# Performance work log

Measured on AMD Instinct MI355X. Metric: run time of the kernel, lower is better.

Reference implementation:

```python
import jax, jax.numpy as jnp
import numpy as np

B, T, P, D = 32, 8, 196, 768
M = 10
NUM_CLASSES = 100
NUM_IDX = 98
P_MASK = 0.5


def setup_inputs() -> dict:
    key = jax.random.key(0)
    ks = jax.random.split(key, 16)
    s = 0.02
    inp = {
        'visual': jax.random.normal(ks[0], (B, T * P, D), jnp.float32),
        'audio': jax.random.normal(ks[1], (B, D), jnp.float32),
        'causal': jax.random.normal(ks[2], (B, M, D), jnp.float32),
        'random_mask': jax.random.uniform(ks[3], (B, T, P, D)) < P_MASK,
        'Wa': jax.random.normal(ks[4], (D, D), jnp.float32) * s,
        'ba': jnp.zeros((D,), jnp.float32),
        'Wv': jax.random.normal(ks[5], (D, D), jnp.float32) * s,
        'bv': jnp.zeros((D,), jnp.float32),
        'Waa': jax.random.normal(ks[6], (D, D), jnp.float32) * s,
        'baa': jnp.zeros((D,), jnp.float32),
        'Wav': jax.random.normal(ks[7], (D, D), jnp.float32) * s,
        'bav': jnp.zeros((D,), jnp.float32),
        'Wf': jax.random.normal(ks[8], (D, D), jnp.float32) * s,
        'bf': jnp.zeros((D,), jnp.float32),
        'Wf2': jax.random.normal(ks[9], (D, 1), jnp.float32) * s,
        'bf2': jnp.zeros((1,), jnp.float32),
        'Wc': jax.random.normal(ks[10], (D, NUM_CLASSES), jnp.float32) * s,
        'bc': jnp.zeros((NUM_CLASSES,), jnp.float32),
        'causal_param': jnp.zeros((1,), jnp.float32),
    }
    return inp


def reference(visual, audio, causal, random_mask, Wa, ba, Wv, bv, Waa, baa,
              Wav, bav, Wf, bf, Wf2, bf2, Wc, bc, causal_param):
    vis = visual.reshape(visual.shape[0], T, -1, D)  # [B,8,196,768]

    # causal_intervention_mean_feature4
    cp = jax.nn.sigmoid(causal_param)                 # soft_clamp2, [1]
    feats = causal @ Wf + bf                          # [B,M,D]
    feats2 = jnp.swapaxes(causal @ Wf2 + bf2, 1, 2)   # [B,1,M]
    fw = jax.nn.softmax(jnp.tanh(feats), axis=1)      # [B,M,D]
    ci = jnp.einsum('bom,bmd->bd', feats2, fw * causal)  # bmm + squeeze
    audio2 = cp * ci + audio                          # [B,D]

    # audio_visual_attention1
    pa = jnp.tanh(audio2 @ Waa + baa)                 # [B,D]
    pv = jnp.tanh(vis @ Wav + bav)                    # [B,T,P,D]
    sscore = pv * pa[:, None, None, :]                # einsum ijkd,id->ijkd
    sattn = jax.nn.softmax(sscore, axis=2)            # softmax over patches
    patch = jnp.sum(sattn, axis=-1)                   # [B,T,P]
    thresh = jnp.sort(patch, axis=-1)[:, :, NUM_IDX]  # per (b,t) threshold
    spa_mask = patch < thresh[:, :, None]             # [B,T,P]
    final_mask = ~(spa_mask[..., None] & random_mask) # [B,T,P,D]
    sfilt = jnp.where(final_mask, sattn, 0.0)

    sav = jnp.sum(sfilt * pv, axis=2)                 # [B,T,D]
    tattn = jax.nn.softmax(sav * pa[:, None, :], axis=1)

    vp = jnp.sum(sfilt * vis, axis=2)                 # [B,T,D]
    vp = jnp.sum(tattn * vp, axis=1)                  # [B,D]

    af = jax.nn.relu(audio2 @ Wa + ba)
    vf = jax.nn.relu(vp @ Wv + bv)
    logits = (af + vf) @ Wc + bc                      # [B,num_classes]
    return logits
```

## Files before the change

kernel.cpp:

```cpp
#include <hip/hip_runtime.h>
#include <hip/hip_bf16.h>
#include <hip/hip_fp16.h>
#include <math.h>

#define BB 32
#define TT 8
#define PP 196
#define DD 768
#define MM 10
#define NCLS 100
#define NIDX 98

typedef __attribute__((ext_vector_type(8))) short short8v;
typedef __attribute__((ext_vector_type(4))) float float4v;

__device__ __forceinline__ float fast_tanh(float x) {
    float e = __expf(2.0f * x);
    return 1.0f - 2.0f / (e + 1.0f);
}
__device__ __forceinline__ unsigned short f2bf(float x) {
    __hip_bfloat16 h = __float2bfloat16(x);
    return *(unsigned short*)&h;
}
__device__ __forceinline__ float bf2f(unsigned short h) {
    return __uint_as_float(((unsigned)h) << 16);
}
__device__ __forceinline__ unsigned short f2h(float x) {
    __half h = __float2half(x);
    return *(unsigned short*)&h;
}
__device__ __forceinline__ float h2f(unsigned short u) {
    __half h = *(__half*)&u;
    return __half2float(h);
}

__global__ __launch_bounds__(768) void k_prep_all(
    const float* __restrict__ vis, unsigned short* __restrict__ visb,
    const unsigned int* __restrict__ rm, int* __restrict__ mode,
    const float* __restrict__ Wav, unsigned short* __restrict__ Wht,
    const float* __restrict__ causal, const float* __restrict__ Wf,
    const float* __restrict__ Wf2,
    float* __restrict__ pf, float* __restrict__ pf2) {
    int t = threadIdx.x;
    int bid = blockIdx.x;
    if (bid < 1024) {
        const size_t NC = (size_t)BB * TT * PP * DD / 8;
        size_t gid = (size_t)bid * 768 + t;
        for (size_t i = gid; i < NC; i += 1024 * 768) {
            const float4* s = (const float4*)(vis + i * 8);
            float4 x = s[0], y = s[1];
            __hip_bfloat162 h;
            unsigned int u0, u1, u2, u3;
            h = __float22bfloat162_rn(make_float2(x.x, x.y)); u0 = *(unsigned int*)&h;
            h = __float22bfloat162_rn(make_float2(x.z, x.w)); u1 = *(unsigned int*)&h;
            h = __float22bfloat162_rn(make_float2(y.x, y.y)); u2 = *(unsigned int*)&h;
            h = __float22bfloat162_rn(make_float2(y.z, y.w)); u3 = *(unsigned int*)&h;
            uint4 o; o.x = u0; o.y = u1; o.z = u2; o.w = u3;
            ((uint4*)visb)[i] = o;
        }
        if (bid == 0) {
            __shared__ int f_ni, f_nf;
            if (t == 0) { f_ni = 0; f_nf = 0; }
            __syncthreads();
            int ni = 0, nf = 0;
            for (int i = t; i < 16384; i += 768) {
                unsigned int v = rm[i];
                ni |= (v > 1u) ? 1 : 0;
                nf |= (v != 0u && v != 0x3F800000u) ? 1 : 0;
            }
            if (ni) atomicOr(&f_ni, 1);
            if (nf) atomicOr(&f_nf, 1);
            __syncthreads();
            if (t == 0) *mode = f_ni ? (f_nf ? 2 : 1) : 0;
        }
    } else if (bid < 1600) {
        __shared__ float tile[32][33];
        int bb = bid - 1024;
        int bn = (bb % 24) * 32;
        int bk = (bb / 24) * 32;
        if (t < 256) {
            int tx = t & 31, ty = t >> 5;
            #pragma unroll
            for (int i = 0; i < 4; ++i)
                tile[ty + i * 8][tx] = Wav[(size_t)(bk + ty + i * 8) * DD + bn + tx];
        }
        __syncthreads();
        if (t < 256) {
            int tx = t & 31, ty = t >> 5;
            #pragma unroll
            for (int i = 0; i < 4; ++i) {
                int n = bn + ty + i * 8, k = bk + tx;
                Wht[(size_t)n * DD + k] = f2bf(tile[tx][ty + i * 8]);
            }
        }
    } else {
        __shared__ float cs[MM][256];
        __shared__ float red[MM][12];
        int bb = bid - 1600;
        int b = bb % 32, kc = bb / 32;
        int k0 = kc * 256;
        for (int i = t; i < MM * 256; i += 768)
            cs[i >> 8][i & 255] = causal[((size_t)b * MM + (i >> 8)) * DD + k0 + (i & 255)];
        __syncthreads();
        int wave = t >> 6, lane = t & 63;
        float w2v = (t < 256) ? Wf2[k0 + t] : 0.f;
        #pragma unroll
        for (int m = 0; m < MM; ++m) {
            float p = (t < 256) ? cs[m][t] * w2v : 0.f;
            #pragma unroll
            for (int o = 32; o > 0; o >>= 1) p += __shfl_down(p, o);
            if (lane == 0) red[m][wave] = p;
        }
        __syncthreads();
        if (t < MM) {
            float s = 0.f;
            #pragma unroll
            for (int wv = 0; wv < 4; ++wv) s += red[t][wv];
            pf2[(b * 3 + kc) * MM + t] = s;
        }
        float acc[MM];
        #pragma unroll
        for (int m = 0; m < MM; ++m) acc[m] = 0.f;
        #pragma unroll 4
        for (int k = 0; k < 256; ++k) {
            float wv = Wf[(size_t)(k0 + k) * DD + t];
            #pragma unroll
            for (int m = 0; m < MM; ++m) acc[m] = fmaf(cs[m][k], wv, acc[m]);
        }
        #pragma unroll
        for (int m = 0; m < MM; ++m)
            pf[(((size_t)b * 3 + kc) * MM + m) * DD + t] = acc[m];
    }
}

__global__ __launch_bounds__(768) void k_audio2a(
    const float* __restrict__ causal, const float* __restrict__ audio,
    const float* __restrict__ pf, const float* __restrict__ pf2,
    const float* __restrict__ bf, const float* __restrict__ bf2,
    const float* __restrict__ cparam, float* __restrict__ a2) {
    int b = blockIdx.x;
    int t = threadIdx.x;
    float cp = 1.0f / (1.0f + __expf(-cparam[0]));
    float tf[MM], f2[MM];
    float mx = -1e30f;
    #pragma unroll
    for (int m = 0; m < MM; ++m) {
        float acc = bf[t];
        float s2 = bf2[0];
        #pragma unroll
        for (int kc = 0; kc < 3; ++kc) {
            acc += pf[(((size_t)b * 3 + kc) * MM + m) * DD + t];
            s2 += pf2[(b * 3 + kc) * MM + m];
        }
        tf[m] = fast_tanh(acc);
        f2[m] = s2;
        mx = fmaxf(mx, tf[m]);
    }
    float s = 0.f;
    #pragma unroll
    for (int m = 0; m < MM; ++m) { tf[m] = __expf(tf[m] - mx); s += tf[m]; }
    float inv = 1.0f / s;
    float ci = 0.f;
    #pragma unroll
    for (int m = 0; m < MM; ++m)
        ci += f2[m] * (tf[m] * inv) * causal[((size_t)b * MM + m) * DD + t];
    a2[(size_t)b * DD + t] = cp * ci + audio[(size_t)b * DD + t];
}

__global__ __launch_bounds__(256) void k_audio2b(
    const float* __restrict__ a2,
    const float* __restrict__ Waa, const float* __restrict__ baa,
    const float* __restrict__ Wa, const float* __restrict__ ba,
    float* __restrict__ pa, float* __restrict__ af, float* __restrict__ colsum) {
    int gid0 = (blockIdx.y * 24 + blockIdx.x) * 256 + threadIdx.x;
    for (int i = gid0; i < BB * TT * DD; i += 48 * 256) colsum[i] = 0.f;
    __shared__ float a2s[16][DD + 4];
    int sel = blockIdx.y;
    const float* W = sel ? Wa : Waa;
    int t = threadIdx.x;
    int c = blockIdx.x * 32 + (t & 31);
    int slot = t >> 5;
    float bias = sel ? ba[c] : baa[c];
    #pragma unroll
    for (int g = 0; g < 2; ++g) {
        if (g) __syncthreads();
        for (int i = t; i < 16 * DD; i += 256)
            a2s[i / DD][i % DD] = a2[(size_t)(g * 16 + i / DD) * DD + i % DD];
        __syncthreads();
        float acc0 = 0.f, acc1 = 0.f;
        #pragma unroll 8
        for (int k = 0; k < DD; ++k) {
            float wv = W[(size_t)k * DD + c];
            acc0 = fmaf(a2s[slot][k], wv, acc0);
            acc1 = fmaf(a2s[slot + 8][k], wv, acc1);
        }
        int b0 = g * 16 + slot, b1 = b0 + 8;
        if (sel == 0) {
            pa[(size_t)b0 * DD + c] = fast_tanh(acc0 + bias);
            pa[(size_t)b1 * DD + c] = fast_tanh(acc1 + bias);
        } else {
            af[(size_t)b0 * DD + c] = fmaxf(acc0 + bias, 0.f);
            af[(size_t)b1 * DD + c] = fmaxf(acc1 + bias, 0.f);
        }
    }
}

__global__ __launch_bounds__(256, 4) void k_pv_mfma(
    const unsigned short* __restrict__ visb, const unsigned short* __restrict__ Wht,
    const float* __restrict__ bav, const float* __restrict__ pa,
    unsigned short* __restrict__ pvh, float* __restrict__ colsum)
{
    __shared__ unsigned short SH[4][4096];
    __shared__ float cred[256];
    int wg = blockIdx.x;
    int lin = (wg & 7) * 294 + (wg >> 3);
    int mt = lin / 6, nt = lin % 6;
    int i0 = mt * 128, n0 = nt * 128;
    int t = threadIdx.x, w = t >> 6, l = t & 63;
    int wm = (w >> 1) * 64, wn = (w & 1) * 64;

    float4v zero4 = {0.f, 0.f, 0.f, 0.f};
    float4v acc[4][4];
    #pragma unroll
    for (int a = 0; a < 4; ++a)
        #pragma unroll
        for (int b = 0; b < 4; ++b) acc[a][b] = zero4;

    int srow[2], scs[2];
    #pragma unroll
    for (int j = 0; j < 2; ++j) {
        int row = (w * 2 + j) * 16 + (l >> 2);
        srow[j] = row;
        scs[j] = (l & 3) ^ ((row >> 1) & 3);
    }

#define STAGE(bb, wnd_)                                                          \
    {                                                                            \
        int kw_ = (wnd_) * 32;                                                   \
        _Pragma("unroll")                                                        \
        for (int j = 0; j < 2; ++j) {                                            \
            size_t aoff_ = (size_t)(i0 + srow[j]) * DD + kw_ + scs[j] * 8;       \
            __builtin_amdgcn_global_load_lds(                                    \
                (const __attribute__((address_space(1))) unsigned int*)(visb + aoff_), \
                (__attribute__((address_space(3))) unsigned int*)&SH[bb][(w * 2 + j) * 512], \
                16, 0, 0);                                                       \
            size_t boff_ = (size_t)(n0 + srow[j]) * DD + kw_ + scs[j] * 8;       \
            __builtin_amdgcn_global_load_lds(                                    \
                (const __attribute__((address_space(1))) unsigned int*)(Wht + boff_), \
                (__attribute__((address_space(3))) unsigned int*)&SH[2 + bb][(w * 2 + j) * 512], \
                16, 0, 0);                                                       \
        }                                                                        \
    }

    STAGE(0, 0);
    for (int wnd = 0; wnd < 24; ++wnd) {
        int cur = wnd & 1;
        if (wnd < 23) {
            STAGE(cur ^ 1, wnd + 1);
            asm volatile("s_waitcnt vmcnt(4)" ::: "memory");
        } else {
            asm volatile("s_waitcnt vmcnt(0)" ::: "memory");
        }
        __builtin_amdgcn_s_barrier();
        __builtin_amdgcn_s_setprio(1);
        {
            short8v ahf[4], bhf[4];
            int cA = l >> 4;
            #pragma unroll
            for (int mr = 0; mr < 4; ++mr) {
                int row = wm + mr * 16 + (l & 15);
                ahf[mr] = *(const short8v*)&SH[cur][row * 32 + ((cA ^ ((row >> 1) & 3)) * 8)];
            }
            #pragma unroll
            for (int nc = 0; nc < 4; ++nc) {
                int row = wn + nc * 16 + (l & 15);
                bhf[nc] = *(const short8v*)&SH[2 + cur][row * 32 + ((cA ^ ((row >> 1) & 3)) * 8)];
            }
            #pragma unroll
            for (int mr = 0; mr < 4; ++mr)
                #pragma unroll
                for (int nc = 0; nc < 4; ++nc)
                    acc[mr][nc] = __builtin_amdgcn_mfma_f32_16x16x32_bf16(
                        ahf[mr], bhf[nc], acc[mr][nc], 0, 0, 0);
        }
        __builtin_amdgcn_s_setprio(0);
        asm volatile("s_waitcnt lgkmcnt(0)" ::: "memory");
        __builtin_amdgcn_sched_barrier(0);
        __builtin_amdgcn_s_barrier();
    }
#undef STAGE
    unsigned short* Cl = &SH[0][0];
    if (t < 256) cred[t] = 0.f;
    __syncthreads();
    int bt0 = i0 / PP;
    int btbound = (bt0 + 1) * PP;
    #pragma unroll
    for (int nc = 0; nc < 4; ++nc) {
        int cl = wn + nc * 16 + (l & 15);
        int col = n0 + cl;
        float bias = bav[col];
        #pragma unroll
        for (int mr = 0; mr < 4; ++mr) {
            int lr0 = wm + mr * 16 + ((l >> 4) << 2);
            int row0 = i0 + lr0;
            int bq = row0 / (TT * PP);
            float pav = pa[(size_t)bq * DD + col];
            float esum = 0.f;
            #pragma unroll
            for (int v = 0; v < 4; ++v) {
                unsigned short pb = f2h(fast_tanh(acc[mr][nc][v] + bias));
                int lr = lr0 + v;
                int boff = lr * 256 + ((cl * 2) ^ ((lr & 7) << 4));
                *(unsigned short*)((char*)Cl + boff) = pb;
                esum += __expf(h2f(pb) * pav);
            }
            int btg = (row0 >= btbound) ? 1 : 0;
            atomicAdd(&cred[btg * 128 + cl], esum);
        }
    }
    __syncthreads();
    #pragma unroll
    for (int rb = 0; rb < 2; ++rb) {
        int lr = (t >> 2) + rb * 64;
        size_t grow = (size_t)(i0 + lr) * DD + n0;
        #pragma unroll
        for (int q = 0; q < 4; ++q) {
            int ch = (t & 3) + q * 4;
            int boff = lr * 256 + ((ch * 16) ^ ((lr & 7) << 4));
            uint4 val = *(uint4*)((char*)Cl + boff);
            *(uint4*)(pvh + grow + ch * 8) = val;
        }
    }
    if (t < 256) {
        int btg = t >> 7, cl = t & 127;
        if (btg == 0 || btbound < i0 + 128)
            atomicAdd(&colsum[(size_t)(bt0 + btg) * DD + n0 + cl], cred[t]);
    }
}

__global__ __launch_bounds__(768) void k_patchsum(
    const unsigned short* __restrict__ pvh, const float* __restrict__ pa,
    const float* __restrict__ colsum, float* __restrict__ patch_q) {
    int bt = blockIdx.x, qd = blockIdx.y;
    int b = bt >> 3;
    size_t base = (size_t)bt * PP * DD;
    int c0 = qd * 192;
    __shared__ float2 pi[192];
    int t = threadIdx.x;
    if (t < 192) {
        int col = c0 + t;
        pi[t] = make_float2(pa[(size_t)b * DD + col],
                            1.0f / colsum[(size_t)bt * DD + col]);
    }
    __syncthreads();
    int wv = t >> 6, l = t & 63;
    for (int p = wv; p < PP; p += 12) {
        float sum = 0.f;
        if (l < 48) {
            const uint2* rv = (const uint2*)(pvh + base + (size_t)p * DD + c0);
            uint2 v = rv[l];
            int c = l * 4;
            float2 q0 = pi[c], q1 = pi[c + 1], q2 = pi[c + 2], q3 = pi[c + 3];
            sum = __expf(h2f((unsigned short)(v.x & 0xFFFFu)) * q0.x) * q0.y
                + __expf(h2f((unsigned short)(v.x >> 16)) * q1.x) * q1.y
                + __expf(h2f((unsigned short)(v.y & 0xFFFFu)) * q2.x) * q2.y
                + __expf(h2f((unsigned short)(v.y >> 16)) * q3.x) * q3.y;
        }
        #pragma unroll
        for (int o = 32; o > 0; o >>= 1) sum += __shfl_down(sum, o);
        if (l == 0) patch_q[((size_t)bt * PP + p) * 4 + qd] = sum;
    }
}

__global__ __launch_bounds__(768) void k_masked(
    const unsigned short* __restrict__ pvh, const unsigned short* __restrict__ visb,
    const void* __restrict__ rmask, const int* __restrict__ mode_p,
    const float* __restrict__ pa, const float* __restrict__ colsum,
    const float* __restrict__ patch_q,
    float* __restrict__ sav, float* __restrict__ vpt) {
    int bt = blockIdx.x;
    int qd = blockIdx.y;
    int b = bt >> 3;
    size_t base = (size_t)bt * PP * DD;
    __shared__ float patch[PP];
    __shared__ unsigned char spa[PP];
    __shared__ float red_s[4][192];
    __shared__ float red_v[4][192];
    int t = threadIdx.x;
    if (t < PP) {
        float4 v = *(const float4*)&patch_q[((size_t)bt * PP + t) * 4];
        patch[t] = ((v.x + v.y) + v.z) + v.w;
    }
    __syncthreads();
    if (t < PP) {
        float x = patch[t];
        int c = 0;
        for (int q = 0; q < PP; ++q) c += (patch[q] <= x) ? 1 : 0;
        spa[t] = (c <= NIDX) ? 1 : 0;
    }
    int pg = t / 192;
    int c = t - pg * 192;
    int col = qd * 192 + c;
    int p0 = pg * 49, p1 = p0 + 49;
    float pav = pa[(size_t)b * DD + col];
    float inv = 1.0f / colsum[(size_t)bt * DD + col];
    __syncthreads();
    const unsigned short* pvb = pvh + base + col;
    const unsigned short* vib = visb + base + col;
    float sava = 0.f, vpa = 0.f;
    int mode = *mode_p;
    if (mode == 0) {
        const int* mb = (const int*)rmask + base + col;
        #pragma unroll 7
        for (int p = p0; p < p1; ++p) {
            float pvv = h2f(pvb[(size_t)p * DD]);
            float sa = __expf(pvv * pav) * inv;
            bool km = !(spa[p] && (mb[(size_t)p * DD] != 0));
            if (km) { sava = fmaf(sa, pvv, sava); vpa = fmaf(sa, bf2f(vib[(size_t)p * DD]), vpa); }
        }
    } else if (mode == 1) {
        const float* mb = (const float*)rmask + base + col;
        #pragma unroll 7
        for (int p = p0; p < p1; ++p) {
            float pvv = h2f(pvb[(size_t)p * DD]);
            float sa = __expf(pvv * pav) * inv;
            bool km = !(spa[p] && (mb[(size_t)p * DD] != 0.f));
            if (km) { sava = fmaf(sa, pvv, sava); vpa = fmaf(sa, bf2f(vib[(size_t)p * DD]), vpa); }
        }
    } else {
        const unsigned char* mb = (const unsigned char*)rmask + base + col;
        #pragma unroll 7
        for (int p = p0; p < p1; ++p) {
            float pvv = h2f(pvb[(size_t)p * DD]);
            float sa = __expf(pvv * pav) * inv;
            bool km = !(spa[p] && (mb[(size_t)p * DD] != 0));
            if (km) { sava = fmaf(sa, pvv, sava); vpa = fmaf(sa, bf2f(vib[(size_t)p * DD]), vpa); }
        }
    }
    red_s[pg][c] = sava;
    red_v[pg][c] = vpa;
    __syncthreads();
    if (t < 192) {
        int col2 = qd * 192 + t;
        sav[(size_t)bt * DD + col2] = red_s[0][t] + red_s[1][t] + red_s[2][t] + red_s[3][t];
        vpt[(size_t)bt * DD + col2] = red_v[0][t] + red_v[1][t] + red_v[2][t] + red_v[3][t];
    }
}

__global__ __launch_bounds__(768) void k_tail(
    const float* __restrict__ sav, const float* __restrict__ vpt,
    const float* __restrict__ pa, const float* __restrict__ af,
    const float* __restrict__ Wv, const float* __restrict__ bv,
    const float* __restrict__ Wc, const float* __restrict__ bc,
    float* __restrict__ out) {
    int b = blockIdx.x;
    int t = threadIdx.x;
    __shared__ float vp[DD];
    __shared__ float h[DD];
    float pav = pa[(size_t)b * DD + t];
    float x[TT];
    float mx = -1e30f;
    #pragma unroll
    for (int k = 0; k < TT; ++k) {
        x[k] = sav[((size_t)b * TT + k) * DD + t] * pav;
        mx = fmaxf(mx, x[k]);
    }
    float s = 0.f;
    #pragma unroll
    for (int k = 0; k < TT; ++k) { x[k] = __expf(x[k] - mx); s += x[k]; }
    float inv = 1.0f / s;
    float acc = 0.f;
    #pragma unroll
    for (int k = 0; k < TT; ++k)
        acc += x[k] * inv * vpt[((size_t)b * TT + k) * DD + t];
    vp[t] = acc;
    __syncthreads();
    float accv = bv[t];
    #pragma unroll 8
    for (int k = 0; k < DD; ++k) accv = fmaf(vp[k], Wv[(size_t)k * DD + t], accv);
    h[t] = fmaxf(accv, 0.f) + af[(size_t)b * DD + t];
    __syncthreads();
    if (t < NCLS) {
        float accc = bc[t];
        #pragma unroll 8
        for (int k = 0; k < DD; ++k) accc = fmaf(h[k], Wc[(size_t)k * NCLS + t], accc);
        out[(size_t)b * NCLS + t] = accc;
    }
}

extern "C" void kernel_launch(void* const* d_in, const int* in_sizes, int n_in,
                              void* d_out, int out_size, void* d_ws, size_t ws_size,
                              hipStream_t stream) {
    const float* visual = (const float*)d_in[0];
    const float* audio  = (const float*)d_in[1];
    const float* causal = (const float*)d_in[2];
    const void*  rmask  = d_in[3];
    const float* Wa   = (const float*)d_in[4];
    const float* ba   = (const float*)d_in[5];
    const float* Wv   = (const float*)d_in[6];
    const float* bv   = (const float*)d_in[7];
    const float* Waa  = (const float*)d_in[8];
    const float* baa  = (const float*)d_in[9];
    const float* Wav  = (const float*)d_in[10];
    const float* bav  = (const float*)d_in[11];
    const float* Wf   = (const float*)d_in[12];
    const float* bf   = (const float*)d_in[13];
    const float* Wf2  = (const float*)d_in[14];
    const float* bf2  = (const float*)d_in[15];
    const float* Wc   = (const float*)d_in[16];
    const float* bc   = (const float*)d_in[17];
    const float* cpar = (const float*)d_in[18];
    float* out = (float*)d_out;

    const size_t NE = (size_t)BB * TT * PP * DD;
    unsigned short* Wht = (unsigned short*)d_ws;
    float* pfreg = (float*)(Wht + (size_t)DD * DD);
    float* colsum = pfreg;
    float* savw  = colsum + (size_t)BB * TT * DD;
    float* vptw  = savw + (size_t)BB * TT * DD;
    float* pf    = pfreg;
    float* pf2   = pfreg + (size_t)BB * 3 * MM * DD;
    float* a2w   = pf2 + 1024;
    float* paw   = a2w + (size_t)BB * DD;
    float* afw   = paw + (size_t)BB * DD;
    int*   modew = (int*)(afw + (size_t)BB * DD);
    unsigned short* visb = (unsigned short*)(modew + 16);
    unsigned short* pvh  = visb + NE;
    float* patchq = (float*)(pvh + NE);

    k_prep_all<<<1696, 768, 0, stream>>>(visual, visb, (const unsigned int*)rmask,
                                         modew, Wav, Wht, causal, Wf, Wf2, pf, pf2);
    k_audio2a<<<BB, 768, 0, stream>>>(causal, audio, pf, pf2, bf, bf2, cpar, a2w);
    k_audio2b<<<dim3(24, 2), 256, 0, stream>>>(a2w, Waa, baa, Wa, ba, paw, afw, colsum);
    k_pv_mfma<<<2352, 256, 0, stream>>>(visb, Wht, bav, paw, pvh, colsum);
    k_patchsum<<<dim3(BB * TT, 4), 768, 0, stream>>>(pvh, paw, colsum, patchq);
    k_masked<<<dim3(BB * TT, 4), 768, 0, stream>>>(pvh, visb, rmask, modew, paw,
                                                   colsum, patchq, savw, vptw);
    k_tail<<<BB, 768, 0, stream>>>(savw, vptw, paw, afw, Wv, bv, Wc, bc, out);
}
```

Baseline: 479.5 us.

## Fuse fp32-to-bf16 visual conversion into GEMM A-operand register loads

Removes the separate pass that converted the visual tensor to bf16. The GEMM now loads fp32 A tiles directly into registers from global memory, converts them in registers, and prefetches the next window, while only the weight operand is staged through LDS. The masked-reduction kernel reads fp32 visual directly. This saves a full read-convert-write pass over the large tensor, but doubles the A-operand bytes the GEMM loads from global memory and raises register pressure. It also doubles the visual bytes read by the masked kernel.

```diff
diff --git a/kernel.cpp b/kernel.cpp
--- a/kernel.cpp
+++ b/kernel.cpp
@@ -22,9 +22,6 @@
     __hip_bfloat16 h = __float2bfloat16(x);
     return *(unsigned short*)&h;
 }
-__device__ __forceinline__ float bf2f(unsigned short h) {
-    return __uint_as_float(((unsigned)h) << 16);
-}
 __device__ __forceinline__ unsigned short f2h(float x) {
     __half h = __float2half(x);
     return *(unsigned short*)&h;
@@ -35,7 +32,6 @@
 }
 
 __global__ __launch_bounds__(768) void k_prep_all(
-    const float* __restrict__ vis, unsigned short* __restrict__ visb,
     const unsigned int* __restrict__ rm, int* __restrict__ mode,
     const float* __restrict__ Wav, unsigned short* __restrict__ Wht,
     const float* __restrict__ causal, const float* __restrict__ Wf,
@@ -43,21 +39,7 @@
     float* __restrict__ pf, float* __restrict__ pf2) {
     int t = threadIdx.x;
     int bid = blockIdx.x;
-    if (bid < 1024) {
-        const size_t NC = (size_t)BB * TT * PP * DD / 8;
-        size_t gid = (size_t)bid * 768 + t;
-        for (size_t i = gid; i < NC; i += 1024 * 768) {
-            const float4* s = (const float4*)(vis + i * 8);
-            float4 x = s[0], y = s[1];
-            __hip_bfloat162 h;
-            unsigned int u0, u1, u2, u3;
-            h = __float22bfloat162_rn(make_float2(x.x, x.y)); u0 = *(unsigned int*)&h;
-            h = __float22bfloat162_rn(make_float2(x.z, x.w)); u1 = *(unsigned int*)&h;
-            h = __float22bfloat162_rn(make_float2(y.x, y.y)); u2 = *(unsigned int*)&h;
-            h = __float22bfloat162_rn(make_float2(y.z, y.w)); u3 = *(unsigned int*)&h;
-            uint4 o; o.x = u0; o.y = u1; o.z = u2; o.w = u3;
-            ((uint4*)visb)[i] = o;
-        }
+    if (bid < 576) {
         if (bid == 0) {
             __shared__ int f_ni, f_nf;
             if (t == 0) { f_ni = 0; f_nf = 0; }
@@ -73,11 +55,9 @@
             __syncthreads();
             if (t == 0) *mode = f_ni ? (f_nf ? 2 : 1) : 0;
         }
-    } else if (bid < 1600) {
         __shared__ float tile[32][33];
-        int bb = bid - 1024;
-        int bn = (bb % 24) * 32;
-        int bk = (bb / 24) * 32;
+        int bn = (bid % 24) * 32;
+        int bk = (bid / 24) * 32;
         if (t < 256) {
             int tx = t & 31, ty = t >> 5;
             #pragma unroll
@@ -96,7 +76,7 @@
     } else {
         __shared__ float cs[MM][256];
         __shared__ float red[MM][12];
-        int bb = bid - 1600;
+        int bb = bid - 576;
         int b = bb % 32, kc = bb / 32;
         int k0 = kc * 256;
         for (int i = t; i < MM * 256; i += 768)
@@ -206,11 +186,11 @@
 }
 
 __global__ __launch_bounds__(256, 4) void k_pv_mfma(
-    const unsigned short* __restrict__ visb, const unsigned short* __restrict__ Wht,
+    const float* __restrict__ vis, const unsigned short* __restrict__ Wht,
     const float* __restrict__ bav, const float* __restrict__ pa,
     unsigned short* __restrict__ pvh, float* __restrict__ colsum)
 {
-    __shared__ unsigned short SH[4][4096];
+    __shared__ unsigned short SH[16384];
     __shared__ float cred[256];
     int wg = blockIdx.x;
     int lin = (wg & 7) * 294 + (wg >> 3);
@@ -226,55 +206,75 @@
         #pragma unroll
         for (int b = 0; b < 4; ++b) acc[a][b] = zero4;
 
-    int srow[2], scs[2];
+    int brow[2], bcs[2];
     #pragma unroll
     for (int j = 0; j < 2; ++j) {
-        int row = (w * 2 + j) * 16 + (l >> 2);
-        srow[j] = row;
-        scs[j] = (l & 3) ^ ((row >> 1) & 3);
-    }
-
-#define STAGE(bb, wnd_)                                                          \
+        int row = j * 64 + (t >> 2);
+        brow[j] = row;
+        bcs[j] = (t & 3) ^ ((row >> 1) & 3);
+    }
+    const float* aptrs[4];
+    #pragma unroll
+    for (int mr = 0; mr < 4; ++mr) {
+        int row = i0 + wm + mr * 16 + (l & 15);
+        aptrs[mr] = vis + (size_t)row * DD + (l >> 4) * 8;
+    }
+    float fA[4][8];
+
+#define LOADA(wnd_)                                                              \
+    {                                                                            \
+        int off_ = (wnd_) * 32;                                                  \
+        _Pragma("unroll")                                                        \
+        for (int mr = 0; mr < 4; ++mr) {                                         \
+            *(float4*)&fA[mr][0] = *(const float4*)(aptrs[mr] + off_);           \
+            *(float4*)&fA[mr][4] = *(const float4*)(aptrs[mr] + off_ + 4);       \
+        }                                                                        \
+    }
+#define STAGEB(bb, wnd_)                                                         \
     {                                                                            \
         int kw_ = (wnd_) * 32;                                                   \
         _Pragma("unroll")                                                        \
         for (int j = 0; j < 2; ++j) {                                            \
-            size_t aoff_ = (size_t)(i0 + srow[j]) * DD + kw_ + scs[j] * 8;       \
-            __builtin_amdgcn_global_load_lds(                                    \
-                (const __attribute__((address_space(1))) unsigned int*)(visb + aoff_), \
-                (__attribute__((address_space(3))) unsigned int*)&SH[bb][(w * 2 + j) * 512], \
-                16, 0, 0);                                                       \
-            size_t boff_ = (size_t)(n0 + srow[j]) * DD + kw_ + scs[j] * 8;       \
+            size_t boff_ = (size_t)(n0 + brow[j]) * DD + kw_ + bcs[j] * 8;       \
             __builtin_amdgcn_global_load_lds(                                    \
                 (const __attribute__((address_space(1))) unsigned int*)(Wht + boff_), \
-                (__attribute__((address_space(3))) unsigned int*)&SH[2 + bb][(w * 2 + j) * 512], \
+                (__attribute__((address_space(3))) unsigned int*)&SH[(bb) * 4096 + j * 2048 + t * 8], \
                 16, 0, 0);                                                       \
         }                                                                        \
     }
 
-    STAGE(0, 0);
+    LOADA(0);
+    STAGEB(0, 0);
     for (int wnd = 0; wnd < 24; ++wnd) {
         int cur = wnd & 1;
         if (wnd < 23) {
-            STAGE(cur ^ 1, wnd + 1);
-            asm volatile("s_waitcnt vmcnt(4)" ::: "memory");
+            STAGEB(cur ^ 1, wnd + 1);
+            asm volatile("s_waitcnt vmcnt(2)" ::: "memory");
         } else {
             asm volatile("s_waitcnt vmcnt(0)" ::: "memory");
         }
         __builtin_amdgcn_s_barrier();
         __builtin_amdgcn_s_setprio(1);
+        short8v ahf[4];
+        #pragma unroll
+        for (int mr = 0; mr < 4; ++mr) {
+            unsigned int u[4];
+            #pragma unroll
+            for (int i = 0; i < 4; ++i) {
+                float2 fp = make_float2(fA[mr][2 * i], fA[mr][2 * i + 1]);
+                __hip_bfloat162 h2 = __float22bfloat162_rn(fp);
+                u[i] = *(unsigned int*)&h2;
+            }
+            ahf[mr] = *(short8v*)u;
+        }
+        if (wnd < 23) LOADA(wnd + 1);
         {
-            short8v ahf[4], bhf[4];
+            short8v bhf[4];
             int cA = l >> 4;
-            #pragma unroll
-            for (int mr = 0; mr < 4; ++mr) {
-                int row = wm + mr * 16 + (l & 15);
-                ahf[mr] = *(const short8v*)&SH[cur][row * 32 + ((cA ^ ((row >> 1) & 3)) * 8)];
-            }
             #pragma unroll
             for (int nc = 0; nc < 4; ++nc) {
                 int row = wn + nc * 16 + (l & 15);
-                bhf[nc] = *(const short8v*)&SH[2 + cur][row * 32 + ((cA ^ ((row >> 1) & 3)) * 8)];
+                bhf[nc] = *(const short8v*)&SH[cur * 4096 + row * 32 + ((cA ^ ((row >> 1) & 3)) * 8)];
             }
             #pragma unroll
             for (int mr = 0; mr < 4; ++mr)
@@ -288,8 +288,9 @@
         __builtin_amdgcn_sched_barrier(0);
         __builtin_amdgcn_s_barrier();
     }
-#undef STAGE
-    unsigned short* Cl = &SH[0][0];
+#undef STAGEB
+#undef LOADA
+    unsigned short* Cl = &SH[0];
     if (t < 256) cred[t] = 0.f;
     __syncthreads();
     int bt0 = i0 / PP;
@@ -373,7 +374,7 @@
 }
 
 __global__ __launch_bounds__(768) void k_masked(
-    const unsigned short* __restrict__ pvh, const unsigned short* __restrict__ visb,
+    const unsigned short* __restrict__ pvh, const float* __restrict__ vis,
     const void* __restrict__ rmask, const int* __restrict__ mode_p,
     const float* __restrict__ pa, const float* __restrict__ colsum,
     const float* __restrict__ patch_q,
@@ -406,7 +407,7 @@
     float inv = 1.0f / colsum[(size_t)bt * DD + col];
     __syncthreads();
     const unsigned short* pvb = pvh + base + col;
-    const unsigned short* vib = visb + base + col;
+    const float* vib = vis + base + col;
     float sava = 0.f, vpa = 0.f;
     int mode = *mode_p;
     if (mode == 0) {
@@ -416,7 +417,7 @@
             float pvv = h2f(pvb[(size_t)p * DD]);
             float sa = __expf(pvv * pav) * inv;
             bool km = !(spa[p] && (mb[(size_t)p * DD] != 0));
-            if (km) { sava = fmaf(sa, pvv, sava); vpa = fmaf(sa, bf2f(vib[(size_t)p * DD]), vpa); }
+            if (km) { sava = fmaf(sa, pvv, sava); vpa = fmaf(sa, vib[(size_t)p * DD], vpa); }
         }
     } else if (mode == 1) {
         const float* mb = (const float*)rmask + base + col;
@@ -425,7 +426,7 @@
             float pvv = h2f(pvb[(size_t)p * DD]);
             float sa = __expf(pvv * pav) * inv;
             bool km = !(spa[p] && (mb[(size_t)p * DD] != 0.f));
-            if (km) { sava = fmaf(sa, pvv, sava); vpa = fmaf(sa, bf2f(vib[(size_t)p * DD]), vpa); }
+            if (km) { sava = fmaf(sa, pvv, sava); vpa = fmaf(sa, vib[(size_t)p * DD], vpa); }
         }
     } else {
         const unsigned char* mb = (const unsigned char*)rmask + base + col;
@@ -434,7 +435,7 @@
             float pvv = h2f(pvb[(size_t)p * DD]);
             float sa = __expf(pvv * pav) * inv;
             bool km = !(spa[p] && (mb[(size_t)p * DD] != 0));
-            if (km) { sava = fmaf(sa, pvv, sava); vpa = fmaf(sa, bf2f(vib[(size_t)p * DD]), vpa); }
+            if (km) { sava = fmaf(sa, pvv, sava); vpa = fmaf(sa, vib[(size_t)p * DD], vpa); }
         }
     }
     red_s[pg][c] = sava;
@@ -524,17 +525,16 @@
     float* paw   = a2w + (size_t)BB * DD;
     float* afw   = paw + (size_t)BB * DD;
     int*   modew = (int*)(afw + (size_t)BB * DD);
-    unsigned short* visb = (unsigned short*)(modew + 16);
-    unsigned short* pvh  = visb + NE;
+    unsigned short* pvh  = (unsigned short*)(modew + 16);
     float* patchq = (float*)(pvh + NE);
 
-    k_prep_all<<<1696, 768, 0, stream>>>(visual, visb, (const unsigned int*)rmask,
-                                         modew, Wav, Wht, causal, Wf, Wf2, pf, pf2);
+    k_prep_all<<<672, 768, 0, stream>>>((const unsigned int*)rmask, modew,
+                                        Wav, Wht, causal, Wf, Wf2, pf, pf2);
     k_audio2a<<<BB, 768, 0, stream>>>(causal, audio, pf, pf2, bf, bf2, cpar, a2w);
     k_audio2b<<<dim3(24, 2), 256, 0, stream>>>(a2w, Waa, baa, Wa, ba, paw, afw, colsum);
-    k_pv_mfma<<<2352, 256, 0, stream>>>(visb, Wht, bav, paw, pvh, colsum);
+    k_pv_mfma<<<2352, 256, 0, stream>>>(visual, Wht, bav, paw, pvh, colsum);
     k_patchsum<<<dim3(BB * TT, 4), 768, 0, stream>>>(pvh, paw, colsum, patchq);
-    k_masked<<<dim3(BB * TT, 4), 768, 0, stream>>>(pvh, visb, rmask, modew, paw,
+    k_masked<<<dim3(BB * TT, 4), 768, 0, stream>>>(pvh, visual, rmask, modew, paw,
                                                    colsum, patchq, savw, vptw);
     k_tail<<<BB, 768, 0, stream>>>(savw, vptw, paw, afw, Wv, bv, Wc, bc, out);
 }
```

New measurement: 675.1 us. 1.41x slower.

## Compute masked sums as unmasked totals minus excluded terms in GEMM epilogue

Applied to the files above, without the earlier changes.

The GEMM epilogue now also accumulates the unmasked sums exp(pv*pa)*pv and exp(pv*pa)*vis per (b,t,column) into two new global buffers, which the prep kernel zeroes. The masked kernel then skips patches not selected by the spatial mask and only visits patches that are both spatially selected and randomly masked. It subtracts their contribution from the normalized unmasked totals. This removes about half the loads and exps in the masked pass, but adds extra visb reads and atomics in the GEMM epilogue and uses a subtraction that can lose floating-point precision.

```diff
diff --git a/kernel.cpp b/kernel.cpp
--- a/kernel.cpp
+++ b/kernel.cpp
@@ -40,7 +40,8 @@
     const float* __restrict__ Wav, unsigned short* __restrict__ Wht,
     const float* __restrict__ causal, const float* __restrict__ Wf,
     const float* __restrict__ Wf2,
-    float* __restrict__ pf, float* __restrict__ pf2) {
+    float* __restrict__ pf, float* __restrict__ pf2,
+    float* __restrict__ uzero) {
     int t = threadIdx.x;
     int bid = blockIdx.x;
     if (bid < 1024) {
@@ -58,6 +59,8 @@
             uint4 o; o.x = u0; o.y = u1; o.z = u2; o.w = u3;
             ((uint4*)visb)[i] = o;
         }
+        for (int i = bid * 768 + t; i < 2 * BB * TT * DD; i += 1024 * 768)
+            uzero[i] = 0.f;
         if (bid == 0) {
             __shared__ int f_ni, f_nf;
             if (t == 0) { f_ni = 0; f_nf = 0; }
@@ -208,10 +211,11 @@
 __global__ __launch_bounds__(256, 4) void k_pv_mfma(
     const unsigned short* __restrict__ visb, const unsigned short* __restrict__ Wht,
     const float* __restrict__ bav, const float* __restrict__ pa,
-    unsigned short* __restrict__ pvh, float* __restrict__ colsum)
+    unsigned short* __restrict__ pvh, float* __restrict__ colsum,
+    float* __restrict__ upv, float* __restrict__ uvis)
 {
     __shared__ unsigned short SH[4][4096];
-    __shared__ float cred[256];
+    __shared__ float cred[3][256];
     int wg = blockIdx.x;
     int lin = (wg & 7) * 294 + (wg >> 3);
     int mt = lin / 6, nt = lin % 6;
@@ -290,7 +294,7 @@
     }
 #undef STAGE
     unsigned short* Cl = &SH[0][0];
-    if (t < 256) cred[t] = 0.f;
+    if (t < 256) { cred[0][t] = 0.f; cred[1][t] = 0.f; cred[2][t] = 0.f; }
     __syncthreads();
     int bt0 = i0 / PP;
     int btbound = (bt0 + 1) * PP;
@@ -305,17 +309,25 @@
             int row0 = i0 + lr0;
             int bq = row0 / (TT * PP);
             float pav = pa[(size_t)bq * DD + col];
-            float esum = 0.f;
+            float esum = 0.f, epsum = 0.f, evsum = 0.f;
             #pragma unroll
             for (int v = 0; v < 4; ++v) {
-                unsigned short pb = f2h(fast_tanh(acc[mr][nc][v] + bias));
+                float pvf = fast_tanh(acc[mr][nc][v] + bias);
+                unsigned short pb = f2h(pvf);
+                float pvq = h2f(pb);
                 int lr = lr0 + v;
                 int boff = lr * 256 + ((cl * 2) ^ ((lr & 7) << 4));
                 *(unsigned short*)((char*)Cl + boff) = pb;
-                esum += __expf(h2f(pb) * pav);
+                float e = __expf(pvq * pav);
+                esum += e;
+                epsum = fmaf(e, pvq, epsum);
+                float vv = bf2f(visb[(size_t)(row0 + v) * DD + col]);
+                evsum = fmaf(e, vv, evsum);
             }
             int btg = (row0 >= btbound) ? 1 : 0;
-            atomicAdd(&cred[btg * 128 + cl], esum);
+            atomicAdd(&cred[0][btg * 128 + cl], esum);
+            atomicAdd(&cred[1][btg * 128 + cl], epsum);
+            atomicAdd(&cred[2][btg * 128 + cl], evsum);
         }
     }
     __syncthreads();
@@ -333,8 +345,12 @@
     }
     if (t < 256) {
         int btg = t >> 7, cl = t & 127;
-        if (btg == 0 || btbound < i0 + 128)
-            atomicAdd(&colsum[(size_t)(bt0 + btg) * DD + n0 + cl], cred[t]);
+        if (btg == 0 || btbound < i0 + 128) {
+            size_t gi = (size_t)(bt0 + btg) * DD + n0 + cl;
+            atomicAdd(&colsum[gi], cred[0][t]);
+            atomicAdd(&upv[gi], cred[1][t]);
+            atomicAdd(&uvis[gi], cred[2][t]);
+        }
     }
 }
 
@@ -377,6 +393,7 @@
     const void* __restrict__ rmask, const int* __restrict__ mode_p,
     const float* __restrict__ pa, const float* __restrict__ colsum,
     const float* __restrict__ patch_q,
+    const float* __restrict__ upv, const float* __restrict__ uvis,
     float* __restrict__ sav, float* __restrict__ vpt) {
     int bt = blockIdx.x;
     int qd = blockIdx.y;
@@ -407,43 +424,56 @@
     __syncthreads();
     const unsigned short* pvb = pvh + base + col;
     const unsigned short* vib = visb + base + col;
-    float sava = 0.f, vpa = 0.f;
+    float sub_s = 0.f, sub_v = 0.f;
     int mode = *mode_p;
     if (mode == 0) {
         const int* mb = (const int*)rmask + base + col;
-        #pragma unroll 7
         for (int p = p0; p < p1; ++p) {
+            if (!spa[p]) continue;
             float pvv = h2f(pvb[(size_t)p * DD]);
-            float sa = __expf(pvv * pav) * inv;
-            bool km = !(spa[p] && (mb[(size_t)p * DD] != 0));
-            if (km) { sava = fmaf(sa, pvv, sava); vpa = fmaf(sa, bf2f(vib[(size_t)p * DD]), vpa); }
+            int mv = mb[(size_t)p * DD];
+            if (mv != 0) {
+                float sa = __expf(pvv * pav) * inv;
+                sub_s = fmaf(sa, pvv, sub_s);
+                sub_v = fmaf(sa, bf2f(vib[(size_t)p * DD]), sub_v);
+            }
         }
     } else if (mode == 1) {
         const float* mb = (const float*)rmask + base + col;
-        #pragma unroll 7
         for (int p = p0; p < p1; ++p) {
+            if (!spa[p]) continue;
             float pvv = h2f(pvb[(size_t)p * DD]);
-            float sa = __expf(pvv * pav) * inv;
-            bool km = !(spa[p] && (mb[(size_t)p * DD] != 0.f));
-            if (km) { sava = fmaf(sa, pvv, sava); vpa = fmaf(sa, bf2f(vib[(size_t)p * DD]), vpa); }
+            float mv = mb[(size_t)p * DD];
+            if (mv != 0.f) {
+                float sa = __expf(pvv * pav) * inv;
+                sub_s = fmaf(sa, pvv, sub_s);
+                sub_v = fmaf(sa, bf2f(vib[(size_t)p * DD]), sub_v);
+            }
         }
     } else {
         const unsigned char* mb = (const unsigned char*)rmask + base + col;
-        #pragma unroll 7
         for (int p = p0; p < p1; ++p) {
+            if (!spa[p]) continue;
             float pvv = h2f(pvb[(size_t)p * DD]);
-            float sa = __expf(pvv * pav) * inv;
-            bool km = !(spa[p] && (mb[(size_t)p * DD] != 0));
-            if (km) { sava = fmaf(sa, pvv, sava); vpa = fmaf(sa, bf2f(vib[(size_t)p * DD]), vpa); }
-        }
-    }
-    red_s[pg][c] = sava;
-    red_v[pg][c] = vpa;
+            unsigned char mv = mb[(size_t)p * DD];
+            if (mv != 0) {
+                float sa = __expf(pvv * pav) * inv;
+                sub_s = fmaf(sa, pvv, sub_s);
+                sub_v = fmaf(sa, bf2f(vib[(size_t)p * DD]), sub_v);
+            }
+        }
+    }
+    red_s[pg][c] = sub_s;
+    red_v[pg][c] = sub_v;
     __syncthreads();
     if (t < 192) {
         int col2 = qd * 192 + t;
-        sav[(size_t)bt * DD + col2] = red_s[0][t] + red_s[1][t] + red_s[2][t] + red_s[3][t];
-        vpt[(size_t)bt * DD + col2] = red_v[0][t] + red_v[1][t] + red_v[2][t] + red_v[3][t];
+        size_t gi = (size_t)bt * DD + col2;
+        float inv2 = 1.0f / colsum[gi];
+        float ss = red_s[0][t] + red_s[1][t] + red_s[2][t] + red_s[3][t];
+        float sv = red_v[0][t] + red_v[1][t] + red_v[2][t] + red_v[3][t];
+        sav[gi] = upv[gi] * inv2 - ss;
+        vpt[gi] = uvis[gi] * inv2 - sv;
     }
 }
 
@@ -527,14 +557,18 @@
     unsigned short* visb = (unsigned short*)(modew + 16);
     unsigned short* pvh  = visb + NE;
     float* patchq = (float*)(pvh + NE);
+    float* upvw   = patchq + (size_t)BB * TT * PP * 4;
+    float* uvisw  = upvw + (size_t)BB * TT * DD;
 
     k_prep_all<<<1696, 768, 0, stream>>>(visual, visb, (const unsigned int*)rmask,
-                                         modew, Wav, Wht, causal, Wf, Wf2, pf, pf2);
+                                         modew, Wav, Wht, causal, Wf, Wf2, pf, pf2,
+                                         upvw);
     k_audio2a<<<BB, 768, 0, stream>>>(causal, audio, pf, pf2, bf, bf2, cpar, a2w);
     k_audio2b<<<dim3(24, 2), 256, 0, stream>>>(a2w, Waa, baa, Wa, ba, paw, afw, colsum);
-    k_pv_mfma<<<2352, 256, 0, stream>>>(visb, Wht, bav, paw, pvh, colsum);
+    k_pv_mfma<<<2352, 256, 0, stream>>>(visb, Wht, bav, paw, pvh, colsum, upvw, uvisw);
     k_patchsum<<<dim3(BB * TT, 4), 768, 0, stream>>>(pvh, paw, colsum, patchq);
     k_masked<<<dim3(BB * TT, 4), 768, 0, stream>>>(pvh, visb, rmask, modew, paw,
-                                                   colsum, patchq, savw, vptw);
+                                                   colsum, patchq, upvw, uvisw,
+                                                   savw, vptw);
     k_tail<<<BB, 768, 0, stream>>>(savw, vptw, paw, afw, Wv, bv, Wc, bc, out);
 }
```

Result: slower. 573.5 us (+19.6%).

## Compute masked sums as unmasked totals minus masked-out contributions

Applied to the files above, without the earlier changes.

Patchsum now also accumulates the unmasked per-column sums of exp-weighted pv and visual, reusing its pv read and adding a visual read. The masked kernel then only visits patches selected by the spatial mask and subtracts the contributions where the random mask is also set, applying the normalisation at the end. This skips about half of the patch reads in the masked kernel, in exchange for extra visual traffic in patchsum and divergent branches.

```diff
diff --git a/kernel.cpp b/kernel.cpp
--- a/kernel.cpp
+++ b/kernel.cpp
@@ -339,36 +339,63 @@
 }
 
 __global__ __launch_bounds__(768) void k_patchsum(
-    const unsigned short* __restrict__ pvh, const float* __restrict__ pa,
-    const float* __restrict__ colsum, float* __restrict__ patch_q) {
+    const unsigned short* __restrict__ pvh, const unsigned short* __restrict__ visb,
+    const float* __restrict__ pa, const float* __restrict__ colsum,
+    float* __restrict__ patch_q, float* __restrict__ upv, float* __restrict__ uvis) {
     int bt = blockIdx.x, qd = blockIdx.y;
     int b = bt >> 3;
     size_t base = (size_t)bt * PP * DD;
     int c0 = qd * 192;
     __shared__ float2 pi[192];
+    __shared__ float us[192], vs[192];
     int t = threadIdx.x;
     if (t < 192) {
         int col = c0 + t;
         pi[t] = make_float2(pa[(size_t)b * DD + col],
                             1.0f / colsum[(size_t)bt * DD + col]);
+        us[t] = 0.f; vs[t] = 0.f;
     }
     __syncthreads();
     int wv = t >> 6, l = t & 63;
+    int c = l * 4;
+    float up0 = 0.f, up1 = 0.f, up2 = 0.f, up3 = 0.f;
+    float uv0 = 0.f, uv1 = 0.f, uv2 = 0.f, uv3 = 0.f;
     for (int p = wv; p < PP; p += 12) {
         float sum = 0.f;
         if (l < 48) {
             const uint2* rv = (const uint2*)(pvh + base + (size_t)p * DD + c0);
+            const uint2* rb = (const uint2*)(visb + base + (size_t)p * DD + c0);
             uint2 v = rv[l];
-            int c = l * 4;
+            uint2 wv2 = rb[l];
+            float p0 = h2f((unsigned short)(v.x & 0xFFFFu));
+            float p1 = h2f((unsigned short)(v.x >> 16));
+            float p2 = h2f((unsigned short)(v.y & 0xFFFFu));
+            float p3 = h2f((unsigned short)(v.y >> 16));
             float2 q0 = pi[c], q1 = pi[c + 1], q2 = pi[c + 2], q3 = pi[c + 3];
-            sum = __expf(h2f((unsigned short)(v.x & 0xFFFFu)) * q0.x) * q0.y
-                + __expf(h2f((unsigned short)(v.x >> 16)) * q1.x) * q1.y
-                + __expf(h2f((unsigned short)(v.y & 0xFFFFu)) * q2.x) * q2.y
-                + __expf(h2f((unsigned short)(v.y >> 16)) * q3.x) * q3.y;
+            float e0 = __expf(p0 * q0.x), e1 = __expf(p1 * q1.x);
+            float e2 = __expf(p2 * q2.x), e3 = __expf(p3 * q3.x);
+            sum = e0 * q0.y + e1 * q1.y + e2 * q2.y + e3 * q3.y;
+            up0 = fmaf(e0, p0, up0); up1 = fmaf(e1, p1, up1);
+            up2 = fmaf(e2, p2, up2); up3 = fmaf(e3, p3, up3);
+            uv0 = fmaf(e0, bf2f((unsigned short)(wv2.x & 0xFFFFu)), uv0);
+            uv1 = fmaf(e1, bf2f((unsigned short)(wv2.x >> 16)), uv1);
+            uv2 = fmaf(e2, bf2f((unsigned short)(wv2.y & 0xFFFFu)), uv2);
+            uv3 = fmaf(e3, bf2f((unsigned short)(wv2.y >> 16)), uv3);
         }
         #pragma unroll
         for (int o = 32; o > 0; o >>= 1) sum += __shfl_down(sum, o);
         if (l == 0) patch_q[((size_t)bt * PP + p) * 4 + qd] = sum;
+    }
+    if (l < 48) {
+        atomicAdd(&us[c], up0); atomicAdd(&us[c + 1], up1);
+        atomicAdd(&us[c + 2], up2); atomicAdd(&us[c + 3], up3);
+        atomicAdd(&vs[c], uv0); atomicAdd(&vs[c + 1], uv1);
+        atomicAdd(&vs[c + 2], uv2); atomicAdd(&vs[c + 3], uv3);
+    }
+    __syncthreads();
+    if (t < 192) {
+        upv[(size_t)bt * DD + c0 + t] = us[t];
+        uvis[(size_t)bt * DD + c0 + t] = vs[t];
     }
 }
 
@@ -377,6 +404,7 @@
     const void* __restrict__ rmask, const int* __restrict__ mode_p,
     const float* __restrict__ pa, const float* __restrict__ colsum,
     const float* __restrict__ patch_q,
+    const float* __restrict__ upv, const float* __restrict__ uvis,
     float* __restrict__ sav, float* __restrict__ vpt) {
     int bt = blockIdx.x;
     int qd = blockIdx.y;
@@ -403,47 +431,59 @@
     int col = qd * 192 + c;
     int p0 = pg * 49, p1 = p0 + 49;
     float pav = pa[(size_t)b * DD + col];
-    float inv = 1.0f / colsum[(size_t)bt * DD + col];
     __syncthreads();
     const unsigned short* pvb = pvh + base + col;
     const unsigned short* vib = visb + base + col;
-    float sava = 0.f, vpa = 0.f;
+    float sub_s = 0.f, sub_v = 0.f;
     int mode = *mode_p;
     if (mode == 0) {
         const int* mb = (const int*)rmask + base + col;
-        #pragma unroll 7
         for (int p = p0; p < p1; ++p) {
+            if (!spa[p]) continue;
             float pvv = h2f(pvb[(size_t)p * DD]);
-            float sa = __expf(pvv * pav) * inv;
-            bool km = !(spa[p] && (mb[(size_t)p * DD] != 0));
-            if (km) { sava = fmaf(sa, pvv, sava); vpa = fmaf(sa, bf2f(vib[(size_t)p * DD]), vpa); }
+            int mv = mb[(size_t)p * DD];
+            if (mv != 0) {
+                float e = __expf(pvv * pav);
+                sub_s = fmaf(e, pvv, sub_s);
+                sub_v = fmaf(e, bf2f(vib[(size_t)p * DD]), sub_v);
+            }
         }
     } else if (mode == 1) {
         const float* mb = (const float*)rmask + base + col;
-        #pragma unroll 7
         for (int p = p0; p < p1; ++p) {
+            if (!spa[p]) continue;
             float pvv = h2f(pvb[(size_t)p * DD]);
-            float sa = __expf(pvv * pav) * inv;
-            bool km = !(spa[p] && (mb[(size_t)p * DD] != 0.f));
-            if (km) { sava = fmaf(sa, pvv, sava); vpa = fmaf(sa, bf2f(vib[(size_t)p * DD]), vpa); }
+            float mv = mb[(size_t)p * DD];
+            if (mv != 0.f) {
+                float e = __expf(pvv * pav);
+                sub_s = fmaf(e, pvv, sub_s);
+                sub_v = fmaf(e, bf2f(vib[(size_t)p * DD]), sub_v);
+            }
         }
     } else {
         const unsigned char* mb = (const unsigned char*)rmask + base + col;
-        #pragma unroll 7
         for (int p = p0; p < p1; ++p) {
+            if (!spa[p]) continue;
             float pvv = h2f(pvb[(size_t)p * DD]);
-            float sa = __expf(pvv * pav) * inv;
-            bool km = !(spa[p] && (mb[(size_t)p * DD] != 0));
-            if (km) { sava = fmaf(sa, pvv, sava); vpa = fmaf(sa, bf2f(vib[(size_t)p * DD]), vpa); }
-        }
-    }
-    red_s[pg][c] = sava;
-    red_v[pg][c] = vpa;
+            unsigned char mv = mb[(size_t)p * DD];
+            if (mv != 0) {
+                float e = __expf(pvv * pav);
+                sub_s = fmaf(e, pvv, sub_s);
+                sub_v = fmaf(e, bf2f(vib[(size_t)p * DD]), sub_v);
+            }
+        }
+    }
+    red_s[pg][c] = sub_s;
+    red_v[pg][c] = sub_v;
     __syncthreads();
     if (t < 192) {
         int col2 = qd * 192 + t;
-        sav[(size_t)bt * DD + col2] = red_s[0][t] + red_s[1][t] + red_s[2][t] + red_s[3][t];
-        vpt[(size_t)bt * DD + col2] = red_v[0][t] + red_v[1][t] + red_v[2][t] + red_v[3][t];
+        size_t gi = (size_t)bt * DD + col2;
+        float inv2 = 1.0f / colsum[gi];
+        float ss = red_s[0][t] + red_s[1][t] + red_s[2][t] + red_s[3][t];
+        float sv = red_v[0][t] + red_v[1][t] + red_v[2][t] + red_v[3][t];
+        sav[gi] = (upv[gi] - ss) * inv2;
+        vpt[gi] = (uvis[gi] - sv) * inv2;
     }
 }
 
@@ -527,14 +567,18 @@
     unsigned short* visb = (unsigned short*)(modew + 16);
     unsigned short* pvh  = visb + NE;
     float* patchq = (float*)(pvh + NE);
+    float* upvw   = patchq + (size_t)BB * TT * PP * 4;
+    float* uvisw  = upvw + (size_t)BB * TT * DD;
 
     k_prep_all<<<1696, 768, 0, stream>>>(visual, visb, (const unsigned int*)rmask,
                                          modew, Wav, Wht, causal, Wf, Wf2, pf, pf2);
     k_audio2a<<<BB, 768, 0, stream>>>(causal, audio, pf, pf2, bf, bf2, cpar, a2w);
     k_audio2b<<<dim3(24, 2), 256, 0, stream>>>(a2w, Waa, baa, Wa, ba, paw, afw, colsum);
     k_pv_mfma<<<2352, 256, 0, stream>>>(visb, Wht, bav, paw, pvh, colsum);
-    k_patchsum<<<dim3(BB * TT, 4), 768, 0, stream>>>(pvh, paw, colsum, patchq);
+    k_patchsum<<<dim3(BB * TT, 4), 768, 0, stream>>>(pvh, visb, paw, colsum,
+                                                     patchq, upvw, uvisw);
     k_masked<<<dim3(BB * TT, 4), 768, 0, stream>>>(pvh, visb, rmask, modew, paw,
-                                                   colsum, patchq, savw, vptw);
+                                                   colsum, patchq, upvw, uvisw,
+                                                   savw, vptw);
     k_tail<<<BB, 768, 0, stream>>>(savw, vptw, paw, afw, Wv, bv, Wc, bc, out);
 }
```

After: 493.0 us. +2.8%, slower.
